# Kernel optimization log

Hardware: AMD Instinct MI355X
Metric: run time of the kernel (lower is better)

The kernel has to match this reference:

```python
import jax, jax.numpy as jnp
import numpy as np

H = 768
FF = 3072
NH = 12
DH = H // NH


def setup_inputs() -> dict:
    key = jax.random.key(0)
    ks = jax.random.split(key, 16)
    s = 0.02
    return {
        "latent": jax.random.normal(ks[0], (2, 2048, H), jnp.float32),
        "ln1_w": jnp.ones((H,), jnp.float32),
        "ln1_b": jnp.zeros((H,), jnp.float32),
        "Wq": jax.random.normal(ks[1], (H, H), jnp.float32) * s,
        "bq": jnp.zeros((H,), jnp.float32),
        "Wk": jax.random.normal(ks[2], (H, H), jnp.float32) * s,
        "bk": jnp.zeros((H,), jnp.float32),
        "Wv": jax.random.normal(ks[3], (H, H), jnp.float32) * s,
        "bv": jnp.zeros((H,), jnp.float32),
        "Wo": jax.random.normal(ks[4], (H, H), jnp.float32) * s,
        "bo": jnp.zeros((H,), jnp.float32),
        "ln2_w": jnp.ones((H,), jnp.float32),
        "ln2_b": jnp.zeros((H,), jnp.float32),
        "W1": jax.random.normal(ks[5], (H, FF), jnp.float32) * s,
        "b1": jnp.zeros((FF,), jnp.float32),
        "W2": jax.random.normal(ks[6], (FF, H), jnp.float32) * s,
        "b2": jnp.zeros((H,), jnp.float32),
    }


def _layernorm(x, w, b, eps=1e-6):
    mu = jnp.mean(x, axis=-1, keepdims=True)
    var = jnp.mean(jnp.square(x - mu), axis=-1, keepdims=True)
    return (x - mu) * jax.lax.rsqrt(var + eps) * w + b


def _split_heads(x):  # [B,S,H] -> [B,NH,S,DH]
    B, S, _ = x.shape
    return x.reshape(B, S, NH, DH).transpose(0, 2, 1, 3)


def reference(latent, ln1_w, ln1_b, Wq, bq, Wk, bk, Wv, bv, Wo, bo,
              ln2_w, ln2_b, W1, b1, W2, b2):
    B, S, _ = latent.shape
    # MHSA (dropouts are p=0.0 / eval mode -> identity)
    nx = _layernorm(latent, ln1_w, ln1_b)
    q = _split_heads(nx @ Wq + bq)
    k = _split_heads(nx @ Wk + bk)
    v = _split_heads(nx @ Wv + bv)
    scores = jnp.einsum('bhqd,bhkd->bhqk', q, k) / jnp.sqrt(jnp.float32(DH))
    attn = jax.nn.softmax(scores, axis=-1)
    ctx = jnp.einsum('bhqk,bhkd->bhqd', attn, v)
    ctx = ctx.transpose(0, 2, 1, 3).reshape(B, S, H)
    latent = latent + (ctx @ Wo + bo)
    # FFN (exact erf GELU as in torch nn.GELU default)
    nx = _layernorm(latent, ln2_w, ln2_b)
    h = jax.nn.gelu(nx @ W1 + b1, approximate=False)
    latent = latent + (h @ W2 + b2)
    return latent
```

## Files before the change

kernel.cpp:

```cpp
#include <hip/hip_runtime.h>

#define H 768
#define FF 3072
#define NH 12
#define DH 64
#define SEQ 2048
#define MTOK 4096

typedef __attribute__((ext_vector_type(8))) short short8;
typedef __attribute__((ext_vector_type(4))) float f32x4;

__device__ __forceinline__ f32x4 mfma16(short8 a, short8 b, f32x4 c) {
  return __builtin_amdgcn_mfma_f32_16x16x32_bf16(a, b, c, 0, 0, 0);
}

__device__ __forceinline__ unsigned short f2bf(float f) {
  union { float f; unsigned int u; } c; c.f = f;
  unsigned int u = c.u;
  u += 0x7fffu + ((u >> 16) & 1u);
  return (unsigned short)(u >> 16);
}
__device__ __forceinline__ float bf2f(unsigned short s) {
  union { unsigned int u; float f; } c; c.u = ((unsigned int)s) << 16;
  return c.f;
}
__device__ __forceinline__ unsigned int pk2bf(float lo, float hi) {
  return (unsigned int)f2bf(lo) | ((unsigned int)f2bf(hi) << 16);
}
__device__ __forceinline__ unsigned int pktrunc(float lo, float hi) {
  union { float f; unsigned int u; } a, b; a.f = hi; b.f = lo;
  return __builtin_amdgcn_perm(a.u, b.u, 0x07060302u);
}

__device__ __forceinline__ void gld16(const unsigned short* g, unsigned short* l) {
  __builtin_amdgcn_global_load_lds(
      (const __attribute__((address_space(1))) void*)g,
      (__attribute__((address_space(3))) void*)l, 16, 0, 0);
}

__global__ __launch_bounds__(256) void prep_kernel(
    const float* __restrict__ Wq, const float* __restrict__ Wk,
    const float* __restrict__ Wv, const float* __restrict__ Wo,
    const float* __restrict__ W1, const float* __restrict__ W2,
    unsigned short* __restrict__ WqkvT, unsigned short* __restrict__ WoT,
    unsigned short* __restrict__ W1T, unsigned short* __restrict__ W2T,
    const float* __restrict__ latent, const float* __restrict__ ln1_w,
    const float* __restrict__ ln1_b, unsigned short* __restrict__ nx) {
  int bid = blockIdx.x;
  int tid = threadIdx.x;
  if (bid >= 6912) {
    int row = bid - 6912;
    const float* xr = latent + (size_t)row * H;
    float v0 = xr[tid], v1 = xr[tid + 256], v2 = xr[tid + 512];
    float s = v0 + v1 + v2;
    float ss = v0 * v0 + v1 * v1 + v2 * v2;
#pragma unroll
    for (int off = 32; off > 0; off >>= 1) {
      s += __shfl_down(s, off);
      ss += __shfl_down(ss, off);
    }
    __shared__ float red[8];
    int wave = tid >> 6, lane = tid & 63;
    if (lane == 0) { red[wave] = s; red[4 + wave] = ss; }
    __syncthreads();
    s = red[0] + red[1] + red[2] + red[3];
    ss = red[4] + red[5] + red[6] + red[7];
    float mu = s * (1.0f / H);
    float var = ss * (1.0f / H) - mu * mu;
    float rs = rsqrtf(var + 1e-6f);
    unsigned short* orow = nx + (size_t)row * H;
    orow[tid]       = f2bf((v0 - mu) * rs * ln1_w[tid]       + ln1_b[tid]);
    orow[tid + 256] = f2bf((v1 - mu) * rs * ln1_w[tid + 256] + ln1_b[tid + 256]);
    orow[tid + 512] = f2bf((v2 - mu) * rs * ln1_w[tid + 512] + ln1_b[tid + 512]);
    return;
  }
  const float* in; unsigned short* out; int K, N, t0;
  if (bid < 1728) {
    K = 768; N = 768;
    if (bid < 576)       { in = Wq; out = WqkvT;                       t0 = bid; }
    else if (bid < 1152) { in = Wk; out = WqkvT + (size_t)768 * 768;   t0 = bid - 576; }
    else                 { in = Wv; out = WqkvT + (size_t)1536 * 768;  t0 = bid - 1152; }
  } else if (bid < 2304) { in = Wo; out = WoT; K = 768;  N = 768;  t0 = bid - 1728; }
  else if (bid < 4608)   { in = W1; out = W1T; K = 768;  N = 3072; t0 = bid - 2304; }
  else                   { in = W2; out = W2T; K = 3072; N = 768;  t0 = bid - 4608; }

  __shared__ float tile[32][33];
  int nb = N >> 5;
  int n0 = (t0 % nb) << 5;
  int k0 = (t0 / nb) << 5;
  int tx = tid & 31, ty = tid >> 5;
#pragma unroll
  for (int yy = 0; yy < 4; ++yy)
    tile[ty + yy * 8][tx] = in[(size_t)(k0 + ty + yy * 8) * N + n0 + tx];
  __syncthreads();
#pragma unroll
  for (int yy = 0; yy < 4; ++yy)
    out[(size_t)(n0 + ty + yy * 8) * K + k0 + tx] = f2bf(tile[tx][ty + yy * 8]);
}

__global__ __launch_bounds__(256) void ln_kernel(const float* __restrict__ x,
                                                 const float* __restrict__ w,
                                                 const float* __restrict__ b,
                                                 unsigned short* __restrict__ out) {
  int row = blockIdx.x;
  int tid = threadIdx.x;
  const float* xr = x + (size_t)row * H;
  float v0 = xr[tid], v1 = xr[tid + 256], v2 = xr[tid + 512];
  float s = v0 + v1 + v2;
  float ss = v0 * v0 + v1 * v1 + v2 * v2;
#pragma unroll
  for (int off = 32; off > 0; off >>= 1) {
    s += __shfl_down(s, off);
    ss += __shfl_down(ss, off);
  }
  __shared__ float red[8];
  int wave = tid >> 6, lane = tid & 63;
  if (lane == 0) { red[wave] = s; red[4 + wave] = ss; }
  __syncthreads();
  s = red[0] + red[1] + red[2] + red[3];
  ss = red[4] + red[5] + red[6] + red[7];
  float mu = s * (1.0f / H);
  float var = ss * (1.0f / H) - mu * mu;
  float rs = rsqrtf(var + 1e-6f);
  unsigned short* orow = out + (size_t)row * H;
  orow[tid]       = f2bf((v0 - mu) * rs * w[tid]       + b[tid]);
  orow[tid + 256] = f2bf((v1 - mu) * rs * w[tid + 256] + b[tid + 256]);
  orow[tid + 512] = f2bf((v2 - mu) * rs * w[tid + 512] + b[tid + 512]);
}

enum { MODE_QKV = 0, MODE_RESID = 1, MODE_GELU = 2 };

template <int MODE>
__global__ __launch_bounds__(256) void gemm128(
    const unsigned short* __restrict__ A,
    const unsigned short* __restrict__ Bt,
    int M, int N, int K,
    const float* __restrict__ bias0,
    const float* __restrict__ bias1,
    const float* __restrict__ bias2,
    unsigned short* __restrict__ out_q,
    unsigned short* __restrict__ out_k,
    unsigned short* __restrict__ out_vT,
    unsigned short* __restrict__ out_bf)
{
  const int mb = M >> 7;
  int m0 = (blockIdx.x % mb) << 7;
  int n0 = (blockIdx.x / mb) << 7;
  int tid = threadIdx.x;
  int wave = tid >> 6, lane = tid & 63;
  int quad = lane >> 4, l16 = lane & 15;
  int wm = (wave & 1) << 6;
  int wn = (wave >> 1) << 6;

  __shared__ __align__(16) unsigned short As[128 * 32];
  __shared__ __align__(16) unsigned short Bs[128 * 32];

  f32x4 acc[4][4];
#pragma unroll
  for (int i = 0; i < 4; ++i)
#pragma unroll
    for (int j = 0; j < 4; ++j) acc[i][j] = (f32x4){0.f, 0.f, 0.f, 0.f};

  int srow = lane >> 2;
  int scol = (lane & 3) << 3;
  const unsigned short* gA0 = A + (size_t)(m0 + wave * 32 + srow) * K + scol;
  const unsigned short* gA1 = gA0 + (size_t)16 * K;
  unsigned short* lA0 = &As[(wave * 32) * 32];
  unsigned short* lA1 = &As[(wave * 32 + 16) * 32];
  const unsigned short* gB0 = Bt + (size_t)(n0 + wave * 32 + srow) * K + scol;
  const unsigned short* gB1 = gB0 + (size_t)16 * K;
  unsigned short* lB0 = &Bs[(wave * 32) * 32];
  unsigned short* lB1 = &Bs[(wave * 32 + 16) * 32];

  for (int k0 = 0; k0 < K; k0 += 32) {
    gld16(gA0 + k0, lA0);
    gld16(gA1 + k0, lA1);
    gld16(gB0 + k0, lB0);
    gld16(gB1 + k0, lB1);
    __syncthreads();
    short8 af[4], bfr[4];
#pragma unroll
    for (int t = 0; t < 4; ++t)
      af[t] = *(const short8*)(&As[(wm + t * 16 + l16) * 32 + quad * 8]);
#pragma unroll
    for (int t = 0; t < 4; ++t)
      bfr[t] = *(const short8*)(&Bs[(wn + t * 16 + l16) * 32 + quad * 8]);
#pragma unroll
    for (int i = 0; i < 4; ++i)
#pragma unroll
      for (int j = 0; j < 4; ++j)
        acc[i][j] = mfma16(af[i], bfr[j], acc[i][j]);
    __syncthreads();
  }

#pragma unroll
  for (int mt = 0; mt < 4; ++mt)
#pragma unroll
    for (int nt = 0; nt < 4; ++nt) {
      f32x4 c = acc[mt][nt];
      int m = m0 + wm + mt * 16 + quad * 4;
      int n = n0 + wn + nt * 16 + l16;
      if (MODE == MODE_QKV) {
        int bb = m >> 11, sIdx = m & 2047;
        if (n < 768) {
          float bs = bias0[n];
          int hh = n >> 6, d = n & 63;
          unsigned short* dst = out_q + (((size_t)(bb * NH + hh)) * SEQ + sIdx) * DH + d;
#pragma unroll
          for (int r = 0; r < 4; ++r) dst[r * DH] = f2bf(c[r] + bs);
        } else if (n < 1536) {
          int nn = n - 768;
          float bs = bias1[nn];
          int hh = nn >> 6, d = nn & 63;
          size_t base = (size_t)(bb * NH + hh) * (SEQ * DH)
                      + (size_t)(sIdx >> 5) * 2048 + ((sIdx >> 4) & 1) * 1024
                      + (d >> 5) * 512 + (sIdx & 15) * 32 + (d & 31);
#pragma unroll
          for (int r = 0; r < 4; ++r) out_k[base + r * 32] = f2bf(c[r] + bs);
        } else {
          int nn = n - 1536;
          float bs = bias2[nn];
          int hh = nn >> 6, d = nn & 63;
          size_t base = (size_t)(bb * NH + hh) * (SEQ * DH)
                      + (size_t)(sIdx >> 5) * 2048 + (d >> 4) * 512
                      + ((sIdx >> 3) & 3) * 128 + (d & 15) * 8 + (sIdx & 7);
          uint2 pk;
          pk.x = pk2bf(c[0] + bs, c[1] + bs);
          pk.y = pk2bf(c[2] + bs, c[3] + bs);
          *(uint2*)(out_vT + base) = pk;
        }
      } else {
        float bs = bias0[n];
        unsigned short* op = out_bf + (size_t)m * N + n;
#pragma unroll
        for (int r = 0; r < 4; ++r) {
          float t = c[r] + bs;
          op[(size_t)r * N] = f2bf(0.5f * t * (1.0f + erff(t * 0.70710678118654752f)));
        }
      }
    }
}

__global__ __launch_bounds__(256) void gemm64r(
    const unsigned short* __restrict__ A,
    const unsigned short* __restrict__ Bt,
    int M, int N, int K,
    const float* __restrict__ bias0,
    const float* __restrict__ resid,
    float* __restrict__ out_f)
{
  const int mb = M >> 6;
  int m0 = (blockIdx.x % mb) << 6;
  int n0 = (blockIdx.x / mb) << 6;
  int tid = threadIdx.x;
  int wave = tid >> 6, lane = tid & 63;
  int quad = lane >> 4, l16 = lane & 15;
  int wm = (wave & 1) << 5;
  int wn = (wave >> 1) << 5;

  __shared__ __align__(16) unsigned short As[4][64 * 32];
  __shared__ __align__(16) unsigned short Bs[4][64 * 32];

  f32x4 acc[2][2];
#pragma unroll
  for (int i = 0; i < 2; ++i)
#pragma unroll
    for (int j = 0; j < 2; ++j) acc[i][j] = (f32x4){0.f, 0.f, 0.f, 0.f};

  int srow = lane >> 2;
  int scol = (lane & 3) << 3;
  const unsigned short* gA = A + (size_t)(m0 + wave * 16 + srow) * K + scol;
  const unsigned short* gB = Bt + (size_t)(n0 + wave * 16 + srow) * K + scol;
  unsigned short* lA = &As[0][(wave * 16) * 32];
  unsigned short* lB = &Bs[0][(wave * 16) * 32];
  const int CH = 64 * 32;

  for (int k0 = 0; k0 < K; k0 += 128) {
#pragma unroll
    for (int kc = 0; kc < 4; ++kc) {
      gld16(gA + k0 + kc * 32, lA + kc * CH);
      gld16(gB + k0 + kc * 32, lB + kc * CH);
    }
    __syncthreads();
#pragma unroll
    for (int kc = 0; kc < 4; ++kc) {
      short8 af[2], bfr[2];
#pragma unroll
      for (int t = 0; t < 2; ++t)
        af[t] = *(const short8*)(&As[kc][(wm + t * 16 + l16) * 32 + quad * 8]);
#pragma unroll
      for (int t = 0; t < 2; ++t)
        bfr[t] = *(const short8*)(&Bs[kc][(wn + t * 16 + l16) * 32 + quad * 8]);
#pragma unroll
      for (int i = 0; i < 2; ++i)
#pragma unroll
        for (int j = 0; j < 2; ++j)
          acc[i][j] = mfma16(af[i], bfr[j], acc[i][j]);
    }
    __syncthreads();
  }

#pragma unroll
  for (int mt = 0; mt < 2; ++mt)
#pragma unroll
    for (int nt = 0; nt < 2; ++nt) {
      f32x4 c = acc[mt][nt];
      int m = m0 + wm + mt * 16 + quad * 4;
      int n = n0 + wn + nt * 16 + l16;
      float bs = bias0[n];
      const float* rp = resid + (size_t)m * N + n;
      float* op = out_f + (size_t)m * N + n;
#pragma unroll
      for (int r = 0; r < 4; ++r) op[(size_t)r * N] = rp[(size_t)r * N] + c[r] + bs;
    }
}

__global__ __launch_bounds__(256, 4) void flash_attn_kernel(
    const unsigned short* __restrict__ q,
    const unsigned short* __restrict__ k,
    const unsigned short* __restrict__ vT,
    unsigned short* __restrict__ ctx)
{
  const float CEXP = 0.18033688011112042f;
  int bh = blockIdx.x % 24;
  int qblk = blockIdx.x / 24;
  int b = bh / NH, h = bh % NH;
  int tid = threadIdx.x;
  int wave = tid >> 6, lane = tid & 63;
  int quad = lane >> 4, l16 = lane & 15;
  int qbase = qblk << 5;

  const unsigned short* qp = q + ((size_t)bh * SEQ + qbase) * DH;
  const unsigned short* kbh = k + (size_t)bh * (SEQ * DH);
  const unsigned short* vbh = vT + (size_t)bh * (SEQ * DH);

  short8 qf00 = *(const short8*)(qp + l16 * DH + quad * 8);
  short8 qf01 = *(const short8*)(qp + l16 * DH + 32 + quad * 8);
  short8 qf10 = *(const short8*)(qp + (16 + l16) * DH + quad * 8);
  short8 qf11 = *(const short8*)(qp + (16 + l16) * DH + 32 + quad * 8);

  f32x4 oacc[2][4];
#pragma unroll
  for (int t = 0; t < 2; ++t)
#pragma unroll
    for (int dt = 0; dt < 4; ++dt) oacc[t][dt] = (f32x4){0.f, 0.f, 0.f, 0.f};
  float L[2] = {0.f, 0.f};

  int addrA = ((((2 * quad) & 3) << 4) + l16) << 2;
  int addrB = ((((2 * quad + 1) & 3) << 4) + l16) << 2;
  bool loquad = quad < 2;

  int klin = (l16 * 4 + quad) * 8;
  int vlin = (quad * 16 + l16) * 8;

  int keylo = wave << 9;
  for (int key0 = keylo; key0 < keylo + 512; key0 += 32) {
    int cbase = (key0 >> 5) * 2048;
    short8 ka0 = *(const short8*)(kbh + cbase + klin);
    short8 ka1 = *(const short8*)(kbh + cbase + 512 + klin);
    short8 kb0 = *(const short8*)(kbh + cbase + 1024 + klin);
    short8 kb1 = *(const short8*)(kbh + cbase + 1536 + klin);
    short8 vf0 = *(const short8*)(vbh + cbase + 0 * 512 + vlin);
    short8 vf1 = *(const short8*)(vbh + cbase + 1 * 512 + vlin);
    short8 vf2 = *(const short8*)(vbh + cbase + 2 * 512 + vlin);
    short8 vf3 = *(const short8*)(vbh + cbase + 3 * 512 + vlin);

#pragma unroll
    for (int t = 0; t < 2; ++t) {
      short8 q0 = t ? qf10 : qf00;
      short8 q1 = t ? qf11 : qf01;
      f32x4 s0 = (f32x4){0.f, 0.f, 0.f, 0.f};
      f32x4 s1 = (f32x4){0.f, 0.f, 0.f, 0.f};
      s0 = mfma16(ka0, q0, s0);
      s0 = mfma16(ka1, q1, s0);
      s1 = mfma16(kb0, q0, s1);
      s1 = mfma16(kb1, q1, s1);

      f32x4 p0, p1;
#pragma unroll
      for (int r = 0; r < 4; ++r) {
        p0[r] = __builtin_amdgcn_exp2f(s0[r] * CEXP);
        p1[r] = __builtin_amdgcn_exp2f(s1[r] * CEXP);
      }
      L[t] += (p0[0] + p0[1]) + (p0[2] + p0[3]) + (p1[0] + p1[1]) + (p1[2] + p1[3]);

      int d00 = (int)pktrunc(p0[0], p0[1]);
      int d01 = (int)pktrunc(p0[2], p0[3]);
      int d10 = (int)pktrunc(p1[0], p1[1]);
      int d11 = (int)pktrunc(p1[2], p1[3]);

      int f0a = __builtin_amdgcn_ds_bpermute(addrA, d00);
      int f0b = __builtin_amdgcn_ds_bpermute(addrA, d10);
      int f1a = __builtin_amdgcn_ds_bpermute(addrA, d01);
      int f1b = __builtin_amdgcn_ds_bpermute(addrA, d11);
      int f2a = __builtin_amdgcn_ds_bpermute(addrB, d00);
      int f2b = __builtin_amdgcn_ds_bpermute(addrB, d10);
      int f3a = __builtin_amdgcn_ds_bpermute(addrB, d01);
      int f3b = __builtin_amdgcn_ds_bpermute(addrB, d11);
      union { short8 s; int i[4]; } pf;
      pf.i[0] = loquad ? f0a : f0b;
      pf.i[1] = loquad ? f1a : f1b;
      pf.i[2] = loquad ? f2a : f2b;
      pf.i[3] = loquad ? f3a : f3b;

      oacc[t][0] = mfma16(vf0, pf.s, oacc[t][0]);
      oacc[t][1] = mfma16(vf1, pf.s, oacc[t][1]);
      oacc[t][2] = mfma16(vf2, pf.s, oacc[t][2]);
      oacc[t][3] = mfma16(vf3, pf.s, oacc[t][3]);
    }
  }

#pragma unroll
  for (int t = 0; t < 2; ++t) {
    L[t] += __shfl_xor(L[t], 16);
    L[t] += __shfl_xor(L[t], 32);
  }

  __shared__ float lbuf[4][2][16];
  __shared__ uint2 obuf[4][2][4][64];

  if (lane < 16) {
    lbuf[wave][0][lane] = L[0];
    lbuf[wave][1][lane] = L[1];
  }
#pragma unroll
  for (int t = 0; t < 2; ++t)
#pragma unroll
    for (int dt = 0; dt < 4; ++dt) {
      uint2 pk;
      pk.x = pk2bf(oacc[t][dt][0], oacc[t][dt][1]);
      pk.y = pk2bf(oacc[t][dt][2], oacc[t][dt][3]);
      obuf[wave][t][dt][lane] = pk;
    }
  __syncthreads();

#pragma unroll
  for (int pp = 0; pp < 2; ++pp) {
    int pi = wave * 2 + pp;
    int t = pi >> 2, dt = pi & 3;
    f32x4 sum = (f32x4){0.f, 0.f, 0.f, 0.f};
#pragma unroll
    for (int w = 0; w < 4; ++w) {
      uint2 pk = obuf[w][t][dt][lane];
      sum[0] += bf2f((unsigned short)(pk.x & 0xffff));
      sum[1] += bf2f((unsigned short)(pk.x >> 16));
      sum[2] += bf2f((unsigned short)(pk.y & 0xffff));
      sum[3] += bf2f((unsigned short)(pk.y >> 16));
    }
    float lstar = lbuf[0][t][l16] + lbuf[1][t][l16] + lbuf[2][t][l16] + lbuf[3][t][l16];
    float rinv = 1.0f / lstar;
    uint2 res;
    res.x = pk2bf(sum[0] * rinv, sum[1] * rinv);
    res.y = pk2bf(sum[2] * rinv, sum[3] * rinv);
    unsigned short* crow = ctx + (size_t)(b * SEQ + qbase + t * 16 + l16) * H
                           + h * DH + dt * 16 + quad * 4;
    *(uint2*)crow = res;
  }
}

extern "C" void kernel_launch(void* const* d_in, const int* in_sizes, int n_in,
                              void* d_out, int out_size, void* d_ws, size_t ws_size,
                              hipStream_t stream) {
  const float* latent = (const float*)d_in[0];
  const float* ln1_w = (const float*)d_in[1];
  const float* ln1_b = (const float*)d_in[2];
  const float* Wq = (const float*)d_in[3];
  const float* bq = (const float*)d_in[4];
  const float* Wk = (const float*)d_in[5];
  const float* bk = (const float*)d_in[6];
  const float* Wv = (const float*)d_in[7];
  const float* bv = (const float*)d_in[8];
  const float* Wo = (const float*)d_in[9];
  const float* bo = (const float*)d_in[10];
  const float* ln2_w = (const float*)d_in[11];
  const float* ln2_b = (const float*)d_in[12];
  const float* W1 = (const float*)d_in[13];
  const float* b1 = (const float*)d_in[14];
  const float* W2 = (const float*)d_in[15];
  const float* b2 = (const float*)d_in[16];
  float* out = (float*)d_out;

  char* ws = (char*)d_ws;
  unsigned short* WqkvT = (unsigned short*)ws; ws += (size_t)2304 * 768 * 2;
  unsigned short* WoT   = (unsigned short*)ws; ws += (size_t)768 * 768 * 2;
  unsigned short* W1T   = (unsigned short*)ws; ws += (size_t)3072 * 768 * 2;
  unsigned short* W2T   = (unsigned short*)ws; ws += (size_t)768 * 3072 * 2;
  unsigned short* nx    = (unsigned short*)ws; ws += (size_t)MTOK * H * 2;
  unsigned short* nx2   = (unsigned short*)ws; ws += (size_t)MTOK * H * 2;
  unsigned short* qb    = (unsigned short*)ws; ws += (size_t)MTOK * H * 2;
  unsigned short* kb    = (unsigned short*)ws; ws += (size_t)MTOK * H * 2;
  unsigned short* vTb   = (unsigned short*)ws; ws += (size_t)MTOK * H * 2;
  unsigned short* ctx   = (unsigned short*)ws; ws += (size_t)MTOK * H * 2;
  unsigned short* hbuf  = (unsigned short*)ws; ws += (size_t)MTOK * FF * 2;
  float* x1             = (float*)ws;          ws += (size_t)MTOK * H * 4;

  prep_kernel<<<6912 + MTOK, 256, 0, stream>>>(
      Wq, Wk, Wv, Wo, W1, W2, WqkvT, WoT, W1T, W2T,
      latent, ln1_w, ln1_b, nx);

  gemm128<MODE_QKV><<<32 * 18, 256, 0, stream>>>(
      nx, WqkvT, MTOK, 2304, 768, bq, bk, bv,
      qb, kb, vTb, nullptr);

  flash_attn_kernel<<<24 * 64, 256, 0, stream>>>(qb, kb, vTb, ctx);

  gemm64r<<<64 * 12, 256, 0, stream>>>(
      ctx, WoT, MTOK, 768, 768, bo, latent, x1);

  ln_kernel<<<MTOK, 256, 0, stream>>>(x1, ln2_w, ln2_b, nx2);

  gemm128<MODE_GELU><<<32 * 24, 256, 0, stream>>>(
      nx2, W1T, MTOK, 3072, 768, b1, nullptr, nullptr,
      nullptr, nullptr, nullptr, hbuf);

  gemm64r<<<64 * 12, 256, 0, stream>>>(
      hbuf, W2T, MTOK, 768, 3072, b2, x1, out);
}
```

Before: 278.5 us.

## Replace ds_bpermute P-fragment shuffle with permlane32_swap and permute V key layout

Inside the attention inner loop, the eight ds_bpermute cross-lane shuffles that rearranged softmax probabilities into MFMA B-operand layout are replaced by two permlane32_swap operations. To keep the result correct, the V-transpose store in the QKV GEMM epilogue permutes key indices within each 32-key block so the PV MFMA sees matching key order. This removes LDS-routed permutes and selects from the hot loop. In exchange the V store becomes two 4-byte writes instead of one 8-byte write.

```diff
diff --git a/kernel.cpp b/kernel.cpp
--- a/kernel.cpp
+++ b/kernel.cpp
@@ -9,6 +9,7 @@
 
 typedef __attribute__((ext_vector_type(8))) short short8;
 typedef __attribute__((ext_vector_type(4))) float f32x4;
+typedef __attribute__((ext_vector_type(2))) unsigned int uint2v;
 
 __device__ __forceinline__ f32x4 mfma16(short8 a, short8 b, f32x4 c) {
   return __builtin_amdgcn_mfma_f32_16x16x32_bf16(a, b, c, 0, 0, 0);
@@ -221,13 +222,13 @@
           int nn = n - 1536;
           float bs = bias2[nn];
           int hh = nn >> 6, d = nn & 63;
-          size_t base = (size_t)(bb * NH + hh) * (SEQ * DH)
-                      + (size_t)(sIdx >> 5) * 2048 + (d >> 4) * 512
-                      + ((sIdx >> 3) & 3) * 128 + (d & 15) * 8 + (sIdx & 7);
-          uint2 pk;
-          pk.x = pk2bf(c[0] + bs, c[1] + bs);
-          pk.y = pk2bf(c[2] + bs, c[3] + bs);
-          *(uint2*)(out_vT + base) = pk;
+          int k5 = sIdx & 31;
+          int sa = (k5 & 0x11) | ((k5 & 0x6) << 1) | ((k5 >> 2) & 0x2);
+          size_t cb = (size_t)(bb * NH + hh) * (SEQ * DH)
+                    + (size_t)(sIdx >> 5) * 2048 + (d >> 4) * 512
+                    + (d & 15) * 8 + (size_t)(sa >> 3) * 128;
+          *(unsigned int*)(out_vT + cb + (sa & 7))       = pk2bf(c[0] + bs, c[1] + bs);
+          *(unsigned int*)(out_vT + cb + ((sa & 7) | 4)) = pk2bf(c[2] + bs, c[3] + bs);
         }
       } else {
         float bs = bias0[n];
@@ -346,10 +347,6 @@
     for (int dt = 0; dt < 4; ++dt) oacc[t][dt] = (f32x4){0.f, 0.f, 0.f, 0.f};
   float L[2] = {0.f, 0.f};
 
-  int addrA = ((((2 * quad) & 3) << 4) + l16) << 2;
-  int addrB = ((((2 * quad + 1) & 3) << 4) + l16) << 2;
-  bool loquad = quad < 2;
-
   int klin = (l16 * 4 + quad) * 8;
   int vlin = (quad * 16 + l16) * 8;
 
@@ -384,24 +381,18 @@
       }
       L[t] += (p0[0] + p0[1]) + (p0[2] + p0[3]) + (p1[0] + p1[1]) + (p1[2] + p1[3]);
 
-      int d00 = (int)pktrunc(p0[0], p0[1]);
-      int d01 = (int)pktrunc(p0[2], p0[3]);
-      int d10 = (int)pktrunc(p1[0], p1[1]);
-      int d11 = (int)pktrunc(p1[2], p1[3]);
-
-      int f0a = __builtin_amdgcn_ds_bpermute(addrA, d00);
-      int f0b = __builtin_amdgcn_ds_bpermute(addrA, d10);
-      int f1a = __builtin_amdgcn_ds_bpermute(addrA, d01);
-      int f1b = __builtin_amdgcn_ds_bpermute(addrA, d11);
-      int f2a = __builtin_amdgcn_ds_bpermute(addrB, d00);
-      int f2b = __builtin_amdgcn_ds_bpermute(addrB, d10);
-      int f3a = __builtin_amdgcn_ds_bpermute(addrB, d01);
-      int f3b = __builtin_amdgcn_ds_bpermute(addrB, d11);
-      union { short8 s; int i[4]; } pf;
-      pf.i[0] = loquad ? f0a : f0b;
-      pf.i[1] = loquad ? f1a : f1b;
-      pf.i[2] = loquad ? f2a : f2b;
-      pf.i[3] = loquad ? f3a : f3b;
+      unsigned int d00 = pktrunc(p0[0], p0[1]);
+      unsigned int d01 = pktrunc(p0[2], p0[3]);
+      unsigned int d10 = pktrunc(p1[0], p1[1]);
+      unsigned int d11 = pktrunc(p1[2], p1[3]);
+
+      uint2v rA = __builtin_amdgcn_permlane32_swap(d00, d10, false, false);
+      uint2v rB = __builtin_amdgcn_permlane32_swap(d01, d11, false, false);
+      union { short8 s; unsigned int i[4]; } pf;
+      pf.i[0] = rA[0];
+      pf.i[1] = rA[1];
+      pf.i[2] = rB[0];
+      pf.i[3] = rB[1];
 
       oacc[t][0] = mfma16(vf0, pf.s, oacc[t][0]);
       oacc[t][1] = mfma16(vf1, pf.s, oacc[t][1]);
```

Result: no change. 277.4 us (-0.4%).
